# Performance work log

Hardware: AMD Instinct MI355X
Metric: run time of the kernel (lower is better)

Reference implementation:

```python
import jax, jax.numpy as jnp
import numpy as np
from jax import lax

EPS = 1e-5
B, T, H, L, K = 64, 1024, 12, 120, 5  # batch, seq len, hidden, lstm layers, conv kernel


def _init(key, shape, scale):
    return scale * jax.random.normal(key, shape, dtype=jnp.float32)


def setup_inputs() -> dict:
    key = jax.random.key(0)
    ks = jax.random.split(key, 16)
    return {
        "x": jax.random.normal(ks[0], (B, 6, T), dtype=jnp.float32),
        "conv_acc_w": _init(ks[1], (6, 6, K), 0.3),
        "conv_acc_b": jnp.zeros((6,), jnp.float32),
        "bn1_gamma": jnp.ones((6,), jnp.float32),
        "bn1_beta": jnp.zeros((6,), jnp.float32),
        "conv_ang_w": _init(ks[2], (6, 6, K), 0.3),
        "conv_ang_b": jnp.zeros((6,), jnp.float32),
        "bn2_gamma": jnp.ones((6,), jnp.float32),
        "bn2_beta": jnp.zeros((6,), jnp.float32),
        "attn_w": _init(ks[3], (H, 6), 0.4),
        "attn_b": jnp.zeros((H,), jnp.float32),
        "lstm_wih": _init(ks[4], (L, 4 * H, H), 0.2),
        "lstm_whh": _init(ks[5], (L, 4 * H, H), 0.2),
        "lstm_bih": _init(ks[6], (L, 4 * H), 0.1),
        "lstm_bhh": _init(ks[7], (L, 4 * H), 0.1),
        "lin1_w": _init(ks[8], (H, H), 0.3),
        "lin1_b": jnp.zeros((H,), jnp.float32),
        "lin2_w": _init(ks[9], (H, H), 0.3),
        "lin2_b": jnp.zeros((H,), jnp.float32),
        "mu_w": _init(ks[10], (H, H), 0.3),
        "mu_b": jnp.zeros((H,), jnp.float32),
        "sigma_w": _init(ks[11], (H, H), 0.3),
        "sigma_b": jnp.zeros((H,), jnp.float32),
    }


def _conv1d(x, w, b):
    # x: (B, C, T) valid conv, matches nn.Conv1d
    y = lax.conv_general_dilated(x, w, (1,), "VALID", dimension_numbers=("NCH", "OIH", "NCH"))
    return y + b[None, :, None]


def _batchnorm(x, gamma, beta):
    # training-mode BatchNorm1d: biased batch stats over (N, T)
    mean = jnp.mean(x, axis=(0, 2), keepdims=True)
    var = jnp.var(x, axis=(0, 2), keepdims=True)
    return (x - mean) * lax.rsqrt(var + EPS) * gamma[None, :, None] + beta[None, :, None]


def _lstm_stack(seq_tbh, wih, whh, bias):
    # seq_tbh: (T', B, H); stacked 120-layer LSTM, torch gate order (i, f, g, o)
    b = seq_tbh.shape[1]
    h0 = jnp.zeros((b, H), seq_tbh.dtype)

    def layer(seq, p):
        w_ih, w_hh, bb = p

        def step(carry, xt):
            h, c = carry
            g = xt @ w_ih.T + h @ w_hh.T + bb  # (B, 4H)
            i, f, gg, o = jnp.split(g, 4, axis=-1)
            c_new = jax.nn.sigmoid(f) * c + jax.nn.sigmoid(i) * jnp.tanh(gg)
            h_new = jax.nn.sigmoid(o) * jnp.tanh(c_new)
            return (h_new, c_new), h_new

        (h_T, _), out = lax.scan(step, (h0, h0), seq)
        return out, h_T

    _, h_last = lax.scan(layer, seq_tbh, (wih, whh, bias))
    return h_last  # (L, B, H): final hidden state of every layer


def _forward(x, conv_acc_w, conv_acc_b, bn1_gamma, bn1_beta, conv_ang_w, conv_ang_b,
             bn2_gamma, bn2_beta, attn_w, attn_b, lstm_wih, lstm_whh, lstm_bih, lstm_bhh,
             lin1_w, lin1_b, lin2_w, lin2_b, mu_w, mu_b, sigma_w, sigma_b):
    out_acc = jax.nn.relu(_batchnorm(_conv1d(x, conv_acc_w, conv_acc_b), bn1_gamma, bn1_beta))
    out_ang = jax.nn.relu(_batchnorm(_conv1d(out_acc, conv_ang_w, conv_ang_b), bn2_gamma, bn2_beta))
    feat = jax.nn.relu(jnp.einsum("bct,hc->bth", out_ang, attn_w) + attn_b)  # (B, T-8, H)
    seq = jnp.transpose(feat, (1, 0, 2))  # (T', B, H) time-major for scan
    h_last = _lstm_stack(seq, lstm_wih, lstm_whh, lstm_bih + lstm_bhh)
    h = jnp.transpose(h_last, (1, 0, 2))  # (B, L, H) == hidden_state.permute(1,0,2)
    h = jax.nn.relu(h @ lin1_w.T + lin1_b)
    out = jax.nn.relu(h @ lin2_w.T + lin2_b)
    mu = out @ mu_w.T + mu_b
    log_var = jax.nn.softplus(out @ sigma_w.T + sigma_b)
    return out, mu, log_var


def reference(x, conv_acc_w, conv_acc_b, bn1_gamma, bn1_beta, conv_ang_w, conv_ang_b,
              bn2_gamma, bn2_beta, attn_w, attn_b, lstm_wih, lstm_whh, lstm_bih, lstm_bhh,
              lin1_w, lin1_b, lin2_w, lin2_b, mu_w, mu_b, sigma_w, sigma_b):
    return _forward(x, conv_acc_w, conv_acc_b, bn1_gamma, bn1_beta, conv_ang_w, conv_ang_b,
                    bn2_gamma, bn2_beta, attn_w, attn_b, lstm_wih, lstm_whh, lstm_bih, lstm_bhh,
                    lin1_w, lin1_b, lin2_w, lin2_b, mu_w, mu_b, sigma_w, sigma_b)
```

## Files before the change

kernel.cpp:

```cpp
#include <hip/hip_runtime.h>
#include <math.h>

#define NLAY 120
#define TT   1016
#define NB   64
#define RB   8
#define IRS  32
#define TPB  384
#define BIGF (1 << 20)

typedef float v2f __attribute__((ext_vector_type(2)));

__device__ __forceinline__ float fast_rcp(float x) { return __builtin_amdgcn_rcpf(x); }
__device__ __forceinline__ float fast_sig(float x) { return fast_rcp(1.f + __expf(-x)); }
__device__ __forceinline__ float fast_tanh(float x) { return 1.f - 2.f * fast_rcp(1.f + __expf(2.f * x)); }

__device__ __forceinline__ int poll_ge_ag(const int* p, int tgt, int cur) {
  long g = 0;
  while (cur < tgt) {
    cur = __hip_atomic_load(p, __ATOMIC_RELAXED, __HIP_MEMORY_SCOPE_AGENT);
    if (cur >= tgt) break;
    __builtin_amdgcn_s_sleep(1);
    if (++g > 400000L) break;
  }
  return cur;
}
__device__ __forceinline__ int poll_ge_wg(const int* p, int tgt, int cur) {
  long g = 0;
  while (cur < tgt) {
    cur = __hip_atomic_load(p, __ATOMIC_RELAXED, __HIP_MEMORY_SCOPE_WORKGROUP);
    if (cur >= tgt) break;
    __builtin_amdgcn_s_sleep(1);
    if (++g > 400000L) break;
  }
  return cur;
}

__global__ void k_conv(const float* __restrict__ xin, const float* __restrict__ cw,
                       const float* __restrict__ cb, const float* __restrict__ aff,
                       float* __restrict__ yout, float* __restrict__ stat,
                       int Tin, int Tout, int use_aff)
{
  const int bx = blockIdx.x;
  const int b = bx / 6, co = bx - b * 6;
  const int tid = threadIdx.x;
  __shared__ float wsh[30];
  __shared__ float ssh[6], shsh[6];
  if (tid < 30) wsh[tid] = cw[co * 30 + tid];
  if (tid < 6) {
    ssh[tid]  = use_aff ? aff[tid] : 1.f;
    shsh[tid] = use_aff ? aff[6 + tid] : 0.f;
  }
  __syncthreads();
  const float bias = cb[co];
  float lsum = 0.f, lsq = 0.f;
  for (int t = tid; t < Tout; t += 256) {
    float acc = bias;
#pragma unroll
    for (int ci = 0; ci < 6; ++ci) {
      const float* xr = xin + ((size_t)b * 6 + ci) * Tin + t;
      const float s = ssh[ci], sh = shsh[ci];
#pragma unroll
      for (int k = 0; k < 5; ++k) {
        float v = xr[k];
        if (use_aff) v = fmaxf(fmaf(s, v, sh), 0.f);
        acc += wsh[ci * 5 + k] * v;
      }
    }
    yout[((size_t)b * 6 + co) * Tout + t] = acc;
    lsum += acc; lsq += acc * acc;
  }
  __shared__ float rs[256], rq[256];
  rs[tid] = lsum; rq[tid] = lsq;
  __syncthreads();
  for (int s = 128; s > 0; s >>= 1) {
    if (tid < s) { rs[tid] += rs[tid + s]; rq[tid] += rq[tid + s]; }
    __syncthreads();
  }
  if (tid == 0) { atomicAdd(&stat[co], rs[0]); atomicAdd(&stat[6 + co], rq[0]); }
}

__global__ void k_finalize(const float* __restrict__ stat,
                           const float* __restrict__ gamma, const float* __restrict__ beta,
                           float* __restrict__ aff, float invN)
{
  const int c = threadIdx.x;
  if (c < 6) {
    float mean = stat[c] * invN;
    float var  = stat[6 + c] * invN - mean * mean;
    float sc   = gamma[c] * rsqrtf(var + 1e-5f);
    aff[c]     = sc;
    aff[6 + c] = fmaf(-mean, sc, beta[c]);
  }
}

__global__ void k_attn(const float* __restrict__ y2, const float* __restrict__ aff2,
                       const float* __restrict__ aw, const float* __restrict__ ab,
                       float* __restrict__ seq0)
{
  const int t = blockIdx.x;
  const int tid = threadIdx.x;
  __shared__ float zb[6 * 64];
  if (tid < 384) {
    const int c = tid >> 6, bb = tid & 63;
    float v = y2[((size_t)bb * 6 + c) * TT + t];
    zb[c * 64 + bb] = fmaxf(fmaf(aff2[c], v, aff2[6 + c]), 0.f);
  }
  __syncthreads();
  const int b = tid / 12, j = tid - b * 12;
  float acc = ab[j];
#pragma unroll
  for (int c = 0; c < 6; ++c) acc += aw[j * 6 + c] * zb[c * 64 + b];
  seq0[(size_t)t * 768 + tid] = fmaxf(acc, 0.f);
}

__global__ __launch_bounds__(TPB, 2) void k_lstm(
    const float* __restrict__ wih, const float* __restrict__ whh,
    const float* __restrict__ bih, const float* __restrict__ bhh,
    const float* __restrict__ seq0, float* __restrict__ ring,
    int* __restrict__ prog, int* __restrict__ cons,
    float* __restrict__ hfin)
{
  const int bid  = blockIdx.x;
  const int c    = bid >> 2;
  const int seg  = bid & 3;
  const int tid  = threadIdx.x;
  const int w    = tid >> 6;
  const int lane = tid & 63;
  const int p    = lane / 12;
  const int j    = lane - p * 12;
  const bool act = (p < 5);
  const int pc   = act ? p : 0;
  const int l    = seg * 30 + w * 5 + pc;

  __shared__ __align__(16) float iring[5][IRS][12];
  __shared__ __align__(16) float xring[2][16][12];
  __shared__ __align__(16) float oring[16][12];
  __shared__ int pflag[6];
  __shared__ int cflag[8];
  float* xrf = &xring[0][0][0];

  if (tid < 6) pflag[tid] = 0;
  if (tid < 8) cflag[tid] = 0;
  __syncthreads();

  int ah_addr[12], ax_addr[12];
#pragma unroll
  for (int k = 0; k < 12; ++k) {
    ah_addr[k] = (pc * 12 + k) * 4;
    ax_addr[k] = (((pc > 0) ? pc - 1 : 0) * 12 + k) * 4;
  }

  v2f wx_if[12], wx_go[12], wh_if[12], wh_go[12];
  v2f b_if = (v2f){0.f, 0.f}, b_go = (v2f){0.f, 0.f};
  if (act) {
    const float* wi = wih + l * 576;
    const float* wh = whh + l * 576;
#pragma unroll
    for (int k = 0; k < 12; ++k) {
      wx_if[k] = (v2f){ wi[(j     ) * 12 + k], wi[(j + 12) * 12 + k] };
      wx_go[k] = (v2f){ wi[(j + 24) * 12 + k], wi[(j + 36) * 12 + k] };
      wh_if[k] = (v2f){ wh[(j     ) * 12 + k], wh[(j + 12) * 12 + k] };
      wh_go[k] = (v2f){ wh[(j + 24) * 12 + k], wh[(j + 36) * 12 + k] };
    }
    const float* ba = bih + l * 48;
    const float* bb = bhh + l * 48;
    b_if = (v2f){ ba[j]      + bb[j],      ba[j + 12] + bb[j + 12] };
    b_go = (v2f){ ba[j + 24] + bb[j + 24], ba[j + 36] + bb[j + 36] };
  }

  const int hop_in  = c * 3 + seg - 1;
  const int hop_out = c * 3 + seg;
  const float* rin  = ring + (size_t)((seg > 0) ? hop_in : 0) * (RB * 192);
  float*       rout = ring + (size_t)((seg < 3) ? hop_out : 0) * (RB * 192);
  const bool is_feeder = (w == 0);
  const bool is_tailer = (w == 5) && (seg < 3);

  const int f0 = lane, f1 = lane + 64, f2 = lane + 128;
  const int s0o0 = (f0 / 12) * 768 + (f0 % 12);
  const int s0o1 = (f1 / 12) * 768 + (f1 % 12);
  const int s0o2 = (f2 / 12) * 768 + (f2 % 12);

  auto ld_batch = [&](int m, float* d) {
    if (seg == 0) {
      const float* b = seq0 + (size_t)m * 16 * 768 + c * 12;
      d[0] = b[s0o0]; d[1] = b[s0o1]; d[2] = b[s0o2];
    } else {
      const float* b = rin + (m & (RB - 1)) * 192;
      d[0] = __hip_atomic_load(b + f0, __ATOMIC_RELAXED, __HIP_MEMORY_SCOPE_AGENT);
      d[1] = __hip_atomic_load(b + f1, __ATOMIC_RELAXED, __HIP_MEMORY_SCOPE_AGENT);
      d[2] = __hip_atomic_load(b + f2, __ATOMIC_RELAXED, __HIP_MEMORY_SCOPE_AGENT);
    }
  };

  float pend[3] = {0.f, 0.f, 0.f};
  int kp = 0, kcons = 0;
  if (is_feeder) {
    if (seg > 0) kp = poll_ge_ag(&prog[hop_in], 2, 0);
    float cur[3];
    ld_batch(0, cur);
    ld_batch(1, pend);
    xrf[f0] = cur[0]; xrf[f1] = cur[1]; xrf[f2] = cur[2];
  }

  float cst = 0.f, hn = 0.f;
  int pcache = 0, ccache = 0;

  auto step = [&](int s, bool guard) __attribute__((always_inline)) {
    const int hbits = __float_as_int(hn);
    float hh[12], xx[12];
#pragma unroll
    for (int k = 0; k < 12; ++k)
      xx[k] = __int_as_float(__builtin_amdgcn_ds_bpermute(ax_addr[k], hbits));
#pragma unroll
    for (int k = 0; k < 12; ++k)
      hh[k] = __int_as_float(__builtin_amdgcn_ds_bpermute(ah_addr[k], hbits));
    if (p == 0) {
      const float4* xp = (w == 0)
          ? (const float4*)(xrf + ((s >> 4) & 1) * 192 + (s & 15) * 12)
          : (const float4*)(&iring[w - 1][s & (IRS - 1)][0]);
      float4 a = xp[0], b4 = xp[1], d = xp[2];
      xx[0]=a.x; xx[1]=a.y; xx[2]=a.z; xx[3]=a.w;
      xx[4]=b4.x; xx[5]=b4.y; xx[6]=b4.z; xx[7]=b4.w;
      xx[8]=d.x; xx[9]=d.y; xx[10]=d.z; xx[11]=d.w;
    }

    v2f xifa = b_if, xgoa = b_go;
    v2f xifb = (v2f){0.f,0.f}, xgob = (v2f){0.f,0.f};
    v2f hifa = (v2f){0.f,0.f}, hgoa = (v2f){0.f,0.f};
    v2f hifb = (v2f){0.f,0.f}, hgob = (v2f){0.f,0.f};
#pragma unroll
    for (int k = 0; k < 6; ++k) {
      v2f xk = { xx[k], xx[k] },     xk2 = { xx[k + 6], xx[k + 6] };
      v2f hk = { hh[k], hh[k] },     hk2 = { hh[k + 6], hh[k + 6] };
      xifa = __builtin_elementwise_fma(wx_if[k],     xk,  xifa);
      xifb = __builtin_elementwise_fma(wx_if[k + 6], xk2, xifb);
      xgoa = __builtin_elementwise_fma(wx_go[k],     xk,  xgoa);
      xgob = __builtin_elementwise_fma(wx_go[k + 6], xk2, xgob);
      hifa = __builtin_elementwise_fma(wh_if[k],     hk,  hifa);
      hifb = __builtin_elementwise_fma(wh_if[k + 6], hk2, hifb);
      hgoa = __builtin_elementwise_fma(wh_go[k],     hk,  hgoa);
      hgob = __builtin_elementwise_fma(wh_go[k + 6], hk2, hgob);
    }
    v2f aif = (xifa + hifa) + (xifb + hifb);
    v2f ago = (xgoa + hgoa) + (xgob + hgob);
    float ig = fast_sig(aif.x);
    float fg = fast_sig(aif.y);
    float gg = fast_tanh(ago.x);
    float og = fast_sig(ago.y);

    if (!guard) {
      cst = fg * cst + ig * gg;
      hn  = og * fast_tanh(cst);
      if (p == 4) {
        if (w < 5) iring[w][(s - 4) & (IRS - 1)][j] = hn;
        else if (seg < 3) oring[(s - 4) & 15][j] = hn;
      }
    } else {
      const int t = s - pc;
      const bool run = act && (t >= 0) && (t < TT);
      if (run) {
        cst = fg * cst + ig * gg;
        hn  = og * fast_tanh(cst);
        if (p == 4) {
          if (w < 5) iring[w][t & (IRS - 1)][j] = hn;
          else if (seg < 3) oring[t & 15][j] = hn;
        }
        if (t == TT - 1) hfin[l * 768 + c * 12 + j] = hn;
      }
    }

    if (is_tailer) {
      const int t4 = s - 4;
      if (t4 >= 0 && t4 < TT && (((t4 & 15) == 15) || t4 == TT - 1)) {
        const int m4 = t4 >> 4;
        if (kcons < m4 - (RB - 1) + 1)
          kcons = poll_ge_ag(&cons[hop_out], m4 - RB + 1, kcons);
        const float* orf = &oring[0][0];
        float o0 = orf[f0], o1 = orf[f1], o2 = orf[f2];
        float* d = rout + (m4 & (RB - 1)) * 192;
        __hip_atomic_store(d + f0, o0, __ATOMIC_RELAXED, __HIP_MEMORY_SCOPE_AGENT);
        __hip_atomic_store(d + f1, o1, __ATOMIC_RELAXED, __HIP_MEMORY_SCOPE_AGENT);
        __hip_atomic_store(d + f2, o2, __ATOMIC_RELAXED, __HIP_MEMORY_SCOPE_AGENT);
        if (lane == 0)
          __hip_atomic_store(&prog[hop_out], m4 + 1, __ATOMIC_RELEASE, __HIP_MEMORY_SCOPE_AGENT);
      }
    }
  };

  for (int s4 = 0; s4 < 1024; s4 += 4) {
    if (is_feeder && (s4 & 15) == 0) {
      const int m = s4 >> 4;
      if (m + 1 < NB) {
        float* xd = xrf + ((m + 1) & 1) * 192;
        xd[f0] = pend[0]; xd[f1] = pend[1]; xd[f2] = pend[2];
      }
      if (m + 2 < NB) {
        if (seg > 0 && kp < m + 3) kp = poll_ge_ag(&prog[hop_in], m + 3, kp);
        ld_batch(m + 2, pend);
      }
      if (seg > 0 && lane == 0)
        __hip_atomic_store(&cons[hop_in], m, __ATOMIC_RELAXED, __HIP_MEMORY_SCOPE_AGENT);
    }

    if (w > 0 && s4 < TT) {
      const int tgt = (s4 + 4 < TT) ? (s4 + 4) : TT;
      if (pcache < tgt) {
        pcache = poll_ge_wg(&pflag[w - 1], tgt, pcache);
        asm volatile("" ::: "memory");
      }
    }
    if (w < 5 && s4 >= 36) {
      const int tgt = s4 - 32;
      if (ccache < tgt) {
        ccache = poll_ge_wg(&cflag[w + 1], tgt, ccache);
        asm volatile("" ::: "memory");
      }
    }

    if (s4 >= 4 && s4 < 1012) {
      step(s4 + 0, false); step(s4 + 1, false); step(s4 + 2, false); step(s4 + 3, false);
    } else {
      step(s4 + 0, true);  step(s4 + 1, true);  step(s4 + 2, true);  step(s4 + 3, true);
    }

    if (lane == 0) {
      asm volatile("" ::: "memory");
      if (w < 5)
        __hip_atomic_store(&pflag[w], s4, __ATOMIC_RELAXED, __HIP_MEMORY_SCOPE_WORKGROUP);
      if (w > 0 && s4 + 3 < TT)
        __hip_atomic_store(&cflag[w], s4 + 4, __ATOMIC_RELAXED, __HIP_MEMORY_SCOPE_WORKGROUP);
    }
  }

  if (lane == 0) {
    asm volatile("" ::: "memory");
    if (w < 5) __hip_atomic_store(&pflag[w], BIGF, __ATOMIC_RELAXED, __HIP_MEMORY_SCOPE_WORKGROUP);
    if (w > 0) __hip_atomic_store(&cflag[w], BIGF, __ATOMIC_RELAXED, __HIP_MEMORY_SCOPE_WORKGROUP);
    if (is_feeder && seg > 0)
      __hip_atomic_store(&cons[hop_in], BIGF, __ATOMIC_RELAXED, __HIP_MEMORY_SCOPE_AGENT);
  }
}

__global__ void k_head(const float* __restrict__ hfin,
                       const float* __restrict__ w1, const float* __restrict__ b1,
                       const float* __restrict__ w2, const float* __restrict__ b2,
                       const float* __restrict__ wm, const float* __restrict__ bm,
                       const float* __restrict__ wsg, const float* __restrict__ bsg,
                       float* __restrict__ out)
{
  const int tid = threadIdx.x;
  __shared__ float s1[144], s2[144], sm[144], ss[144];
  __shared__ float v1[12], v2[12], vm[12], vs[12];
  if (tid < 144) { s1[tid] = w1[tid]; s2[tid] = w2[tid]; sm[tid] = wm[tid]; ss[tid] = wsg[tid]; }
  if (tid < 12)  { v1[tid] = b1[tid]; v2[tid] = b2[tid]; vm[tid] = bm[tid]; vs[tid] = bsg[tid]; }
  __syncthreads();
  const int r = blockIdx.x * 256 + tid;
  const int b = r / 120, l = r - b * 120;
  float h[12];
#pragma unroll
  for (int k = 0; k < 12; ++k) h[k] = hfin[l * 768 + b * 12 + k];
  float u1[12];
#pragma unroll
  for (int u = 0; u < 12; ++u) {
    float a = v1[u];
#pragma unroll
    for (int k = 0; k < 12; ++k) a += s1[u * 12 + k] * h[k];
    u1[u] = fmaxf(a, 0.f);
  }
  float u2[12];
#pragma unroll
  for (int u = 0; u < 12; ++u) {
    float a = v2[u];
#pragma unroll
    for (int k = 0; k < 12; ++k) a += s2[u * 12 + k] * u1[k];
    u2[u] = fmaxf(a, 0.f);
  }
  const size_t base = (size_t)r * 12;
#pragma unroll
  for (int u = 0; u < 12; ++u) out[base + u] = u2[u];
#pragma unroll
  for (int u = 0; u < 12; ++u) {
    float a = vm[u];
#pragma unroll
    for (int k = 0; k < 12; ++k) a += sm[u * 12 + k] * u2[k];
    out[92160 + base + u] = a;
  }
#pragma unroll
  for (int u = 0; u < 12; ++u) {
    float a = vs[u];
#pragma unroll
    for (int k = 0; k < 12; ++k) a += ss[u * 12 + k] * u2[k];
    out[184320 + base + u] = fmaxf(a, 0.f) + log1pf(expf(-fabsf(a)));
  }
}

extern "C" void kernel_launch(void* const* d_in, const int* in_sizes, int n_in,
                              void* d_out, int out_size, void* d_ws, size_t ws_size,
                              hipStream_t stream)
{
  const float* x   = (const float*)d_in[0];
  const float* c1w = (const float*)d_in[1];
  const float* c1b = (const float*)d_in[2];
  const float* g1  = (const float*)d_in[3];
  const float* be1 = (const float*)d_in[4];
  const float* c2w = (const float*)d_in[5];
  const float* c2b = (const float*)d_in[6];
  const float* g2  = (const float*)d_in[7];
  const float* be2 = (const float*)d_in[8];
  const float* aw  = (const float*)d_in[9];
  const float* ab  = (const float*)d_in[10];
  const float* wih = (const float*)d_in[11];
  const float* whh = (const float*)d_in[12];
  const float* bih = (const float*)d_in[13];
  const float* bhh = (const float*)d_in[14];
  const float* l1w = (const float*)d_in[15];
  const float* l1b = (const float*)d_in[16];
  const float* l2w = (const float*)d_in[17];
  const float* l2b = (const float*)d_in[18];
  const float* muw = (const float*)d_in[19];
  const float* mub = (const float*)d_in[20];
  const float* sgw = (const float*)d_in[21];
  const float* sgb = (const float*)d_in[22];

  float* ws    = (float*)d_ws;
  float* stat1 = ws;
  float* stat2 = ws + 12;
  float* aff1  = ws + 24;
  float* aff2  = ws + 36;
  int*   prog  = (int*)(ws + 64);
  int*   cons  = (int*)(ws + 304);
  float* y1    = ws + 576;
  float* y2    = y1 + 391680;
  float* seq0  = y2 + 390144;
  float* ring  = seq0 + 780288;
  float* hfin  = ring + (size_t)192 * RB * 192;

  hipMemsetAsync(d_ws, 0, 576 * sizeof(float), stream);

  k_conv<<<384, 256, 0, stream>>>(x, c1w, c1b, nullptr, y1, stat1, 1024, 1020, 0);
  k_finalize<<<1, 64, 0, stream>>>(stat1, g1, be1, aff1, 1.f / 65280.f);
  k_conv<<<384, 256, 0, stream>>>(y1, c2w, c2b, aff1, y2, stat2, 1020, 1016, 1);
  k_finalize<<<1, 64, 0, stream>>>(stat2, g2, be2, aff2, 1.f / 65024.f);
  k_attn<<<1016, 768, 0, stream>>>(y2, aff2, aw, ab, seq0);
  k_lstm<<<256, TPB, 0, stream>>>(wih, whh, bih, bhh, seq0, ring, prog, cons, hfin);
  k_head<<<30, 256, 0, stream>>>(hfin, l1w, l1b, l2w, l2b, muw, mub, sgw, sgb, (float*)d_out);
}
```

Measured before the change: 979.3 us.

## Use fp16 packed dot products and LDS double-buffered hidden exchange in LSTM

LSTM weights are packed to fp16 pairs, and gate pre-activations are computed with fdot2 instead of fp32 packed FMAs, which halves the weight register footprint and the FMA count. The 24 cross-lane bpermutes per step are replaced by a double-buffered fp16 shared-memory hidden-state buffer that each lane reads as packed halves. The cost is reduced precision in the recurrence over 120 stacked layers. It also adds a shared-memory store on every step and relies on the wavefront running in lockstep to keep the double buffer correct.

```diff
diff --git a/kernel.cpp b/kernel.cpp
--- a/kernel.cpp
+++ b/kernel.cpp
@@ -10,6 +10,7 @@
 #define BIGF (1 << 20)
 
 typedef float v2f __attribute__((ext_vector_type(2)));
+typedef __fp16 h2 __attribute__((ext_vector_type(2)));
 
 __device__ __forceinline__ float fast_rcp(float x) { return __builtin_amdgcn_rcpf(x); }
 __device__ __forceinline__ float fast_sig(float x) { return fast_rcp(1.f + __expf(-x)); }
@@ -133,48 +134,45 @@
   const int pc   = act ? p : 0;
   const int l    = seg * 30 + w * 5 + pc;
 
+  __shared__ __align__(16) __fp16 hlocH[6][2][96];
   __shared__ __align__(16) float iring[5][IRS][12];
   __shared__ __align__(16) float xring[2][16][12];
   __shared__ __align__(16) float oring[16][12];
-  __shared__ int pflag[6];
-  __shared__ int cflag[8];
+  __shared__ int pflag[8], cflag[8];
   float* xrf = &xring[0][0][0];
 
-  if (tid < 6) pflag[tid] = 0;
-  if (tid < 8) cflag[tid] = 0;
+  if (tid < 8) { pflag[tid] = 0; cflag[tid] = 0; }
+  {
+    __fp16 z = (__fp16)0.f;
+    hlocH[w][0][lane] = z; hlocH[w][1][lane] = z;
+    hlocH[w][0][64 + (lane & 31)] = z; hlocH[w][1][64 + (lane & 31)] = z;
+  }
   __syncthreads();
 
-  int ah_addr[12], ax_addr[12];
-#pragma unroll
-  for (int k = 0; k < 12; ++k) {
-    ah_addr[k] = (pc * 12 + k) * 4;
-    ax_addr[k] = (((pc > 0) ? pc - 1 : 0) * 12 + k) * 4;
-  }
-
-  v2f wx_if[12], wx_go[12], wh_if[12], wh_go[12];
-  v2f b_if = (v2f){0.f, 0.f}, b_go = (v2f){0.f, 0.f};
+  h2 wx[4][6] = {}, wh2v[4][6] = {};
+  float bias[4] = {0.f, 0.f, 0.f, 0.f};
   if (act) {
     const float* wi = wih + l * 576;
     const float* wh = whh + l * 576;
 #pragma unroll
-    for (int k = 0; k < 12; ++k) {
-      wx_if[k] = (v2f){ wi[(j     ) * 12 + k], wi[(j + 12) * 12 + k] };
-      wx_go[k] = (v2f){ wi[(j + 24) * 12 + k], wi[(j + 36) * 12 + k] };
-      wh_if[k] = (v2f){ wh[(j     ) * 12 + k], wh[(j + 12) * 12 + k] };
-      wh_go[k] = (v2f){ wh[(j + 24) * 12 + k], wh[(j + 36) * 12 + k] };
-    }
-    const float* ba = bih + l * 48;
-    const float* bb = bhh + l * 48;
-    b_if = (v2f){ ba[j]      + bb[j],      ba[j + 12] + bb[j + 12] };
-    b_go = (v2f){ ba[j + 24] + bb[j + 24], ba[j + 36] + bb[j + 36] };
+    for (int q = 0; q < 4; ++q) {
+      const int row = j + 12 * q;
+#pragma unroll
+      for (int kk = 0; kk < 6; ++kk) {
+        wx[q][kk]   = __builtin_amdgcn_cvt_pkrtz(wi[row * 12 + 2 * kk], wi[row * 12 + 2 * kk + 1]);
+        wh2v[q][kk] = __builtin_amdgcn_cvt_pkrtz(wh[row * 12 + 2 * kk], wh[row * 12 + 2 * kk + 1]);
+      }
+      bias[q] = bih[l * 48 + row] + bhh[l * 48 + row];
+    }
   }
 
   const int hop_in  = c * 3 + seg - 1;
   const int hop_out = c * 3 + seg;
-  const float* rin  = ring + (size_t)((seg > 0) ? hop_in : 0) * (RB * 192);
-  float*       rout = ring + (size_t)((seg < 3) ? hop_out : 0) * (RB * 192);
+  const bool has_up = (seg > 0), has_dn = (seg < 3);
+  const float* rin  = ring + (size_t)(has_up ? hop_in : 0) * (RB * 192);
+  float*       rout = ring + (size_t)(has_dn ? hop_out : 0) * (RB * 192);
   const bool is_feeder = (w == 0);
-  const bool is_tailer = (w == 5) && (seg < 3);
+  const bool is_tailer = (w == 5) && has_dn;
 
   const int f0 = lane, f1 = lane + 64, f2 = lane + 128;
   const int s0o0 = (f0 / 12) * 768 + (f0 % 12);
@@ -196,7 +194,7 @@
   float pend[3] = {0.f, 0.f, 0.f};
   int kp = 0, kcons = 0;
   if (is_feeder) {
-    if (seg > 0) kp = poll_ge_ag(&prog[hop_in], 2, 0);
+    if (has_up) kp = poll_ge_ag(&prog[hop_in], 2, 0);
     float cur[3];
     ld_batch(0, cur);
     ld_batch(1, pend);
@@ -207,67 +205,73 @@
   int pcache = 0, ccache = 0;
 
   auto step = [&](int s, bool guard) __attribute__((always_inline)) {
-    const int hbits = __float_as_int(hn);
-    float hh[12], xx[12];
-#pragma unroll
-    for (int k = 0; k < 12; ++k)
-      xx[k] = __int_as_float(__builtin_amdgcn_ds_bpermute(ax_addr[k], hbits));
-#pragma unroll
-    for (int k = 0; k < 12; ++k)
-      hh[k] = __int_as_float(__builtin_amdgcn_ds_bpermute(ah_addr[k], hbits));
+    const int rb = (s & 1) ^ 1, wb = s & 1;
+
+    h2 px[6], ph[6];
+    {
+      const h2* hp = (const h2*)&hlocH[w][rb][pc * 16];
+#pragma unroll
+      for (int kk = 0; kk < 6; ++kk) ph[kk] = hp[kk];
+    }
     if (p == 0) {
       const float4* xp = (w == 0)
           ? (const float4*)(xrf + ((s >> 4) & 1) * 192 + (s & 15) * 12)
           : (const float4*)(&iring[w - 1][s & (IRS - 1)][0]);
       float4 a = xp[0], b4 = xp[1], d = xp[2];
-      xx[0]=a.x; xx[1]=a.y; xx[2]=a.z; xx[3]=a.w;
-      xx[4]=b4.x; xx[5]=b4.y; xx[6]=b4.z; xx[7]=b4.w;
-      xx[8]=d.x; xx[9]=d.y; xx[10]=d.z; xx[11]=d.w;
-    }
-
-    v2f xifa = b_if, xgoa = b_go;
-    v2f xifb = (v2f){0.f,0.f}, xgob = (v2f){0.f,0.f};
-    v2f hifa = (v2f){0.f,0.f}, hgoa = (v2f){0.f,0.f};
-    v2f hifb = (v2f){0.f,0.f}, hgob = (v2f){0.f,0.f};
-#pragma unroll
-    for (int k = 0; k < 6; ++k) {
-      v2f xk = { xx[k], xx[k] },     xk2 = { xx[k + 6], xx[k + 6] };
-      v2f hk = { hh[k], hh[k] },     hk2 = { hh[k + 6], hh[k + 6] };
-      xifa = __builtin_elementwise_fma(wx_if[k],     xk,  xifa);
-      xifb = __builtin_elementwise_fma(wx_if[k + 6], xk2, xifb);
-      xgoa = __builtin_elementwise_fma(wx_go[k],     xk,  xgoa);
-      xgob = __builtin_elementwise_fma(wx_go[k + 6], xk2, xgob);
-      hifa = __builtin_elementwise_fma(wh_if[k],     hk,  hifa);
-      hifb = __builtin_elementwise_fma(wh_if[k + 6], hk2, hifb);
-      hgoa = __builtin_elementwise_fma(wh_go[k],     hk,  hgoa);
-      hgob = __builtin_elementwise_fma(wh_go[k + 6], hk2, hgob);
-    }
-    v2f aif = (xifa + hifa) + (xifb + hifb);
-    v2f ago = (xgoa + hgoa) + (xgob + hgob);
-    float ig = fast_sig(aif.x);
-    float fg = fast_sig(aif.y);
-    float gg = fast_tanh(ago.x);
-    float og = fast_sig(ago.y);
+      px[0] = __builtin_amdgcn_cvt_pkrtz(a.x, a.y);
+      px[1] = __builtin_amdgcn_cvt_pkrtz(a.z, a.w);
+      px[2] = __builtin_amdgcn_cvt_pkrtz(b4.x, b4.y);
+      px[3] = __builtin_amdgcn_cvt_pkrtz(b4.z, b4.w);
+      px[4] = __builtin_amdgcn_cvt_pkrtz(d.x, d.y);
+      px[5] = __builtin_amdgcn_cvt_pkrtz(d.z, d.w);
+    } else {
+      const h2* xp = (const h2*)&hlocH[w][rb][(pc - (pc > 0)) * 16];
+#pragma unroll
+      for (int kk = 0; kk < 6; ++kk) px[kk] = xp[kk];
+    }
+
+    float a0 = bias[0], a1 = bias[1], a2 = bias[2], a3 = bias[3];
+#pragma unroll
+    for (int kk = 0; kk < 6; ++kk) {
+      a0 = __builtin_amdgcn_fdot2(wx[0][kk], px[kk], a0, false);
+      a1 = __builtin_amdgcn_fdot2(wx[1][kk], px[kk], a1, false);
+      a2 = __builtin_amdgcn_fdot2(wx[2][kk], px[kk], a2, false);
+      a3 = __builtin_amdgcn_fdot2(wx[3][kk], px[kk], a3, false);
+    }
+#pragma unroll
+    for (int kk = 0; kk < 6; ++kk) {
+      a0 = __builtin_amdgcn_fdot2(wh2v[0][kk], ph[kk], a0, false);
+      a1 = __builtin_amdgcn_fdot2(wh2v[1][kk], ph[kk], a1, false);
+      a2 = __builtin_amdgcn_fdot2(wh2v[2][kk], ph[kk], a2, false);
+      a3 = __builtin_amdgcn_fdot2(wh2v[3][kk], ph[kk], a3, false);
+    }
+    float ig = fast_sig(a0);
+    float fg = fast_sig(a1);
+    float gv = fast_tanh(a2);
+    float og = fast_sig(a3);
 
     if (!guard) {
-      cst = fg * cst + ig * gg;
+      cst = fg * cst + ig * gv;
       hn  = og * fast_tanh(cst);
+      hlocH[w][wb][p * 16 + j] = (__fp16)hn;
       if (p == 4) {
-        if (w < 5) iring[w][(s - 4) & (IRS - 1)][j] = hn;
-        else if (seg < 3) oring[(s - 4) & 15][j] = hn;
+        const int t = s - 4;
+        if (w < 5) iring[w][t & (IRS - 1)][j] = hn;
+        else if (has_dn) oring[t & 15][j] = hn;
       }
     } else {
       const int t = s - pc;
       const bool run = act && (t >= 0) && (t < TT);
       if (run) {
-        cst = fg * cst + ig * gg;
+        cst = fg * cst + ig * gv;
         hn  = og * fast_tanh(cst);
-        if (p == 4) {
-          if (w < 5) iring[w][t & (IRS - 1)][j] = hn;
-          else if (seg < 3) oring[t & 15][j] = hn;
-        }
-        if (t == TT - 1) hfin[l * 768 + c * 12 + j] = hn;
-      }
+      }
+      hlocH[w][wb][p * 16 + j] = (__fp16)hn;
+      if (p == 4 && t >= 0 && t < TT) {
+        if (w < 5) iring[w][t & (IRS - 1)][j] = hn;
+        else if (has_dn) oring[t & 15][j] = hn;
+      }
+      if (run && t == TT - 1) hfin[l * 768 + c * 12 + j] = hn;
     }
 
     if (is_tailer) {
@@ -296,10 +300,10 @@
         xd[f0] = pend[0]; xd[f1] = pend[1]; xd[f2] = pend[2];
       }
       if (m + 2 < NB) {
-        if (seg > 0 && kp < m + 3) kp = poll_ge_ag(&prog[hop_in], m + 3, kp);
+        if (has_up && kp < m + 3) kp = poll_ge_ag(&prog[hop_in], m + 3, kp);
         ld_batch(m + 2, pend);
       }
-      if (seg > 0 && lane == 0)
+      if (has_up && lane == 0)
         __hip_atomic_store(&cons[hop_in], m, __ATOMIC_RELAXED, __HIP_MEMORY_SCOPE_AGENT);
     }
 
@@ -337,7 +341,7 @@
     asm volatile("" ::: "memory");
     if (w < 5) __hip_atomic_store(&pflag[w], BIGF, __ATOMIC_RELAXED, __HIP_MEMORY_SCOPE_WORKGROUP);
     if (w > 0) __hip_atomic_store(&cflag[w], BIGF, __ATOMIC_RELAXED, __HIP_MEMORY_SCOPE_WORKGROUP);
-    if (is_feeder && seg > 0)
+    if (is_feeder && has_up)
       __hip_atomic_store(&cons[hop_in], BIGF, __ATOMIC_RELAXED, __HIP_MEMORY_SCOPE_AGENT);
   }
 }
@@ -436,7 +440,7 @@
   float* ring  = seq0 + 780288;
   float* hfin  = ring + (size_t)192 * RB * 192;
 
-  hipMemsetAsync(d_ws, 0, 576 * sizeof(float), stream);
+  (void)hipMemsetAsync(d_ws, 0, 576 * sizeof(float), stream);
 
   k_conv<<<384, 256, 0, stream>>>(x, c1w, c1b, nullptr, y1, stat1, 1024, 1020, 0);
   k_finalize<<<1, 64, 0, stream>>>(stat1, g1, be1, aff1, 1.f / 65280.f);
```

After: 857.7 us. -12.4%, faster.
